# Kernel optimization log

Hardware: AMD Instinct MI355X
Metric: run time of the kernel (lower is better)

## Reference

```python
import jax, jax.numpy as jnp
import numpy as np


def toeplitz_from(weight_matrix):
    # Faithful to the torch Toeplitz parametrization:
    # parameters = concat(W[::-1, 0], W[0, 1:]); toep[i, j] = parameters[n_rows-1-i+j]
    n_rows, n_cols = weight_matrix.shape
    params = jnp.concatenate([weight_matrix[::-1, 0], weight_matrix[0, 1:]])
    idx = (n_rows - 1) - jnp.arange(n_rows)[:, None] + jnp.arange(n_cols)[None, :]
    return params[idx]  # [n_rows, n_cols], built in one gather instead of a loop


def setup_inputs() -> dict:
    key = jax.random.key(0)
    ks = jax.random.split(key, 8)
    B, frame_dim, esn_dim, last_dim = 65536, 64, 960, 1024
    comb = frame_dim + esn_dim
    s1 = 1.0 / np.sqrt(comb)
    s2 = 1.0 / np.sqrt(last_dim)
    return {
        "x_frame": jax.random.normal(ks[0], (B, frame_dim), jnp.float32),
        "h_esn": jax.random.normal(ks[1], (B, esn_dim), jnp.float32),
        "W1": jax.random.normal(ks[2], (last_dim, comb), jnp.float32) * s1,
        "b1": jax.random.normal(ks[3], (last_dim,), jnp.float32) * s1,
        "W_slope": jax.random.normal(ks[4], (frame_dim, last_dim), jnp.float32) * s2,
        "b_slope": jax.random.normal(ks[5], (frame_dim,), jnp.float32) * s2,
        "W_int": jax.random.normal(ks[6], (frame_dim, last_dim), jnp.float32) * s2,
        "b_int": jax.random.normal(ks[7], (frame_dim,), jnp.float32) * s2,
    }


def reference(x_frame, h_esn, W1, b1, W_slope, b_slope, W_int, b_int):
    W1_toep = toeplitz_from(W1)                      # [last_dim, frame+esn]
    combined = jnp.concatenate([x_frame, h_esn], axis=-1)  # [B, frame+esn]
    q_last = jax.nn.relu(combined @ W1_toep.T + b1)  # [B, last_dim]
    slope = jnp.tanh(q_last @ W_slope.T + b_slope)   # [B, frame_dim]
    intercept = q_last @ W_int.T + b_int             # [B, frame_dim]
    return slope, intercept
```

## Files before the change

### kernel.cpp

```cpp
#include <hip/hip_runtime.h>
#include <cstdint>
#include <cstddef>

typedef __bf16 bf16x8v __attribute__((ext_vector_type(8)));
typedef float f32x4v __attribute__((ext_vector_type(4)));

__device__ __forceinline__ void gload_lds16(const void* g, void* l) {
  __builtin_amdgcn_global_load_lds((const __attribute__((address_space(1))) void*)g,
                                   (__attribute__((address_space(3))) void*)l,
                                   16, 0, 0);
}

__device__ __forceinline__ bf16x8v cvt_bf16x8(f32x4v a, f32x4v b) {
  bf16x8v r;
  r[0] = (__bf16)a[0]; r[1] = (__bf16)a[1]; r[2] = (__bf16)a[2]; r[3] = (__bf16)a[3];
  r[4] = (__bf16)b[0]; r[5] = (__bf16)b[1]; r[6] = (__bf16)b[2]; r[7] = (__bf16)b[3];
  return r;
}

__global__ __launch_bounds__(256) void params_kernel(const float* __restrict__ W1,
                                                     float* __restrict__ params) {
  int p = blockIdx.x * 256 + threadIdx.x;
  if (p < 2047)
    params[p] = (p < 1024) ? W1[(size_t)(1023 - p) << 10] : W1[p - 1023];
}

__global__ __launch_bounds__(256) void pack_kernel(const float* __restrict__ x,
                                                   const float* __restrict__ h,
                                                   const float* __restrict__ params,
                                                   const float* __restrict__ Ws,
                                                   const float* __restrict__ Wi,
                                                   __bf16* __restrict__ Acat,
                                                   __bf16* __restrict__ toep,
                                                   __bf16* __restrict__ Wcat) {
  long u = (long)blockIdx.x * 256 + threadIdx.x;
  if (u < 8388608L) {
    int r = (int)(u >> 7), cg = (int)(u & 127);
    const float* s = (cg < 8) ? x + (size_t)r * 64 + cg * 8
                              : h + (size_t)r * 960 + (cg - 8) * 8;
    f32x4v a = *(const f32x4v*)s, b = *(const f32x4v*)(s + 4);
    *(bf16x8v*)(Acat + ((size_t)r << 10) + cg * 8) = cvt_bf16x8(a, b);
  } else if (u < 8519680L) {
    long t = u - 8388608L;
    int i = (int)(t >> 7), j0 = (int)(t & 127) * 8;
    const float* s = params + (1023 - i + j0);
    bf16x8v o;
#pragma unroll
    for (int e = 0; e < 8; ++e) o[e] = (__bf16)s[e];
    *(bf16x8v*)(toep + ((size_t)i << 10) + j0) = o;
  } else {
    long t = u - 8519680L;
    int n = (int)(t >> 7), k0 = (int)(t & 127) * 8;
    const float* s = (n < 64) ? Ws + ((size_t)n << 10) + k0
                              : Wi + ((size_t)(n - 64) << 10) + k0;
    f32x4v a = *(const f32x4v*)s, b = *(const f32x4v*)(s + 4);
    *(bf16x8v*)(Wcat + ((size_t)n << 10) + k0) = cvt_bf16x8(a, b);
  }
}

__global__ __launch_bounds__(256) void gemm1_dma(const __bf16* __restrict__ Acat,
                                                 const __bf16* __restrict__ toep,
                                                 const float* __restrict__ b1,
                                                 __bf16* __restrict__ q) {
  __shared__ __align__(16) __bf16 Ab0[128 * 32], Ab1[128 * 32];
  __shared__ __align__(16) __bf16 Bb0[128 * 32], Bb1[128 * 32];
  const int tid = threadIdx.x, wid = tid >> 6, lane = tid & 63;
  const int wrow = wid >> 1, wcol = wid & 1;
  const int bid = blockIdx.x;
  const int xcd = bid & 7, j = bid >> 3;
  const int m0 = (((j >> 3) << 3) | xcd) << 7;
  const int n0 = (j & 7) << 7;
  const int quad = lane >> 4, l15 = lane & 15;
  const int rl = lane >> 2, seg = lane & 3;

  f32x4v acc[4][4] = {};

  const __bf16* gA = Acat + (((size_t)(m0 + wid * 32 + rl)) << 10) + seg * 8;
  const __bf16* gB = toep + (((size_t)(n0 + wid * 32 + rl)) << 10) + seg * 8;
  const size_t ROW16 = (size_t)16 << 10;

  auto stage = [&](__bf16* la, __bf16* lb) {
    int rb = wid * 32;
    gload_lds16(gA,         &la[rb * 32]);
    gload_lds16(gA + ROW16, &la[(rb + 16) * 32]);
    gload_lds16(gB,         &lb[rb * 32]);
    gload_lds16(gB + ROW16, &lb[(rb + 16) * 32]);
    gA += 32; gB += 32;
  };

  auto compute = [&](const __bf16* la, const __bf16* lb) {
    bf16x8v af[4], bfr[4];
#pragma unroll
    for (int r = 0; r < 4; ++r)
      af[r] = *(const bf16x8v*)&la[(wrow * 64 + r * 16 + l15) * 32 + quad * 8];
#pragma unroll
    for (int c = 0; c < 4; ++c)
      bfr[c] = *(const bf16x8v*)&lb[(wcol * 64 + c * 16 + l15) * 32 + quad * 8];
#pragma unroll
    for (int r = 0; r < 4; ++r)
#pragma unroll
      for (int c = 0; c < 4; ++c)
        acc[r][c] = __builtin_amdgcn_mfma_f32_16x16x32_bf16(af[r], bfr[c], acc[r][c], 0, 0, 0);
  };

  stage(Ab0, Bb0);
  for (int kt = 0; kt < 32; kt += 2) {
    __syncthreads();
    stage(Ab1, Bb1);
    compute(Ab0, Bb0);
    __syncthreads();
    if (kt < 30) stage(Ab0, Bb0);
    compute(Ab1, Bb1);
  }

#pragma unroll
  for (int c = 0; c < 4; ++c) {
    int col = n0 + wcol * 64 + c * 16 + l15;
    float bias = b1[col];
#pragma unroll
    for (int r = 0; r < 4; ++r)
#pragma unroll
      for (int e = 0; e < 4; ++e) {
        int row = m0 + wrow * 64 + r * 16 + quad * 4 + e;
        q[((size_t)row << 10) + col] = (__bf16)fmaxf(acc[r][c][e] + bias, 0.0f);
      }
  }
}

__global__ __launch_bounds__(256) void gemm2_dma(const __bf16* __restrict__ q,
                                                 const __bf16* __restrict__ Wcat,
                                                 const float* __restrict__ b_slope,
                                                 const float* __restrict__ b_int,
                                                 float* __restrict__ out) {
  __shared__ __align__(16) __bf16 Ab[2][64 * 64];
  __shared__ __align__(16) __bf16 Bb[2][128 * 64];
  const int tid = threadIdx.x, wid = tid >> 6, lane = tid & 63;
  const int wrow = wid >> 1, wcol = wid & 1;
  const int m0 = blockIdx.x << 6;
  const int quad = lane >> 4, l15 = lane & 15;
  const int r8 = lane >> 3, s8 = lane & 7;

  f32x4v acc[2][4] = {};

  auto stage = [&](int buf, int kt) {
    int k0 = kt << 6;
#pragma unroll
    for (int j = 0; j < 2; ++j) {
      int rb = wid * 16 + j * 8;
      gload_lds16(q + (((size_t)(m0 + rb + r8)) << 10) + k0 + s8 * 8, &Ab[buf][rb * 64]);
    }
#pragma unroll
    for (int j = 0; j < 4; ++j) {
      int rb = wid * 32 + j * 8;
      gload_lds16(Wcat + (((size_t)(rb + r8)) << 10) + k0 + s8 * 8, &Bb[buf][rb * 64]);
    }
  };

  stage(0, 0);
  for (int kt = 0; kt < 16; ++kt) {
    int cur = kt & 1;
    __syncthreads();
    if (kt < 15) stage(cur ^ 1, kt + 1);
#pragma unroll
    for (int s = 0; s < 2; ++s) {
      bf16x8v af[2], bfr[4];
#pragma unroll
      for (int r = 0; r < 2; ++r)
        af[r] = *(const bf16x8v*)&Ab[cur][(wrow * 32 + r * 16 + l15) * 64 + s * 32 + quad * 8];
#pragma unroll
      for (int c = 0; c < 4; ++c)
        bfr[c] = *(const bf16x8v*)&Bb[cur][(wcol * 64 + c * 16 + l15) * 64 + s * 32 + quad * 8];
#pragma unroll
      for (int r = 0; r < 2; ++r)
#pragma unroll
        for (int c = 0; c < 4; ++c)
          acc[r][c] = __builtin_amdgcn_mfma_f32_16x16x32_bf16(af[r], bfr[c], acc[r][c], 0, 0, 0);
    }
  }

#pragma unroll
  for (int c = 0; c < 4; ++c) {
    int col = wcol * 64 + c * 16 + l15;
    float bias = (col < 64) ? b_slope[col] : b_int[col - 64];
#pragma unroll
    for (int r = 0; r < 2; ++r)
#pragma unroll
      for (int e = 0; e < 4; ++e) {
        int row = m0 + wrow * 32 + r * 16 + quad * 4 + e;
        float v = acc[r][c][e] + bias;
        if (col < 64) {
          float xc = fminf(fmaxf(v, -15.f), 15.f);
          float t = __expf(2.f * xc);
          out[(size_t)row * 64 + col] = (t - 1.f) / (t + 1.f);
        } else {
          out[(size_t)4194304 + (size_t)row * 64 + (col - 64)] = v;
        }
      }
  }
}

__global__ __launch_bounds__(256) void gemm1_fused(const float* __restrict__ x,
                                                   const float* __restrict__ h,
                                                   const __bf16* __restrict__ toep,
                                                   const float* __restrict__ b1,
                                                   __bf16* __restrict__ q) {
  __shared__ __align__(16) __bf16 At[128 * 32];
  __shared__ __align__(16) __bf16 Bt[128 * 32];
  const int tid = threadIdx.x, wid = tid >> 6, lane = tid & 63;
  const int wrow = wid >> 1, wcol = wid & 1;
  const int m0 = (blockIdx.x >> 3) << 7;
  const int n0 = (blockIdx.x & 7) << 7;
  const int quad = lane >> 4, l15 = lane & 15;
  const int rl = lane >> 2, seg = lane & 3;

  f32x4v acc[4][4] = {};
  auto a_ptr = [&](int k0, int t) -> const f32x4v* {
    const float* s; int ld, kk;
    if (k0 < 64) { s = x; ld = 64; kk = k0; } else { s = h; ld = 960; kk = k0 - 64; }
    int row = m0 + wid * 32 + t * 16 + rl;
    return (const f32x4v*)(s + (size_t)row * ld + kk + seg * 8);
  };
  f32x4v pv[2][2];
  { const f32x4v* p0 = a_ptr(0, 0); pv[0][0] = p0[0]; pv[0][1] = p0[1];
    const f32x4v* p1 = a_ptr(0, 1); pv[1][0] = p1[0]; pv[1][1] = p1[1]; }

  for (int k0 = 0; k0 < 1024; k0 += 32) {
    __syncthreads();
    { int rb = wid * 32;
#pragma unroll
      for (int c = 0; c < 2; ++c) {
        int row = rb + c * 16 + rl;
        gload_lds16(toep + (((size_t)(n0 + row)) << 10) + k0 + seg * 8, &Bt[(rb + c * 16) * 32]);
      } }
#pragma unroll
    for (int t = 0; t < 2; ++t) {
      int row = wid * 32 + t * 16 + rl;
      *(bf16x8v*)&At[row * 32 + seg * 8] = cvt_bf16x8(pv[t][0], pv[t][1]);
    }
    __syncthreads();
    if (k0 + 32 < 1024) {
      const f32x4v* p0 = a_ptr(k0 + 32, 0); f32x4v n00 = p0[0], n01 = p0[1];
      const f32x4v* p1 = a_ptr(k0 + 32, 1); f32x4v n10 = p1[0], n11 = p1[1];
      pv[0][0] = n00; pv[0][1] = n01; pv[1][0] = n10; pv[1][1] = n11;
    }
    bf16x8v af[4], bfr[4];
#pragma unroll
    for (int r = 0; r < 4; ++r)
      af[r] = *(const bf16x8v*)&At[(wrow * 64 + r * 16 + l15) * 32 + quad * 8];
#pragma unroll
    for (int c = 0; c < 4; ++c)
      bfr[c] = *(const bf16x8v*)&Bt[(wcol * 64 + c * 16 + l15) * 32 + quad * 8];
#pragma unroll
    for (int r = 0; r < 4; ++r)
#pragma unroll
      for (int c = 0; c < 4; ++c)
        acc[r][c] = __builtin_amdgcn_mfma_f32_16x16x32_bf16(af[r], bfr[c], acc[r][c], 0, 0, 0);
  }
#pragma unroll
  for (int c = 0; c < 4; ++c) {
    int col = n0 + wcol * 64 + c * 16 + l15;
    float bias = b1[col];
#pragma unroll
    for (int r = 0; r < 4; ++r)
#pragma unroll
      for (int e = 0; e < 4; ++e) {
        int row = m0 + wrow * 64 + r * 16 + quad * 4 + e;
        q[((size_t)row << 10) + col] = (__bf16)fmaxf(acc[r][c][e] + bias, 0.0f);
      }
  }
}

__global__ __launch_bounds__(256) void prep_kernel(const float* __restrict__ W1,
                                                   const float* __restrict__ Wslope,
                                                   const float* __restrict__ Wint,
                                                   __bf16* __restrict__ toep,
                                                   __bf16* __restrict__ Wcat) {
  int id = blockIdx.x * 256 + threadIdx.x;
  if (id < 1024 * 1024) {
    int i = id >> 10, j = id & 1023;
    int p = 1023 - i + j;
    float v = (p < 1024) ? W1[(size_t)(1023 - p) << 10] : W1[p - 1023];
    toep[id] = (__bf16)v;
  } else {
    int id2 = id - 1024 * 1024;
    int n = id2 >> 10, k = id2 & 1023;
    float v = (n < 64) ? Wslope[((size_t)n << 10) + k] : Wint[((size_t)(n - 64) << 10) + k];
    Wcat[id2] = (__bf16)v;
  }
}

extern "C" void kernel_launch(void* const* d_in, const int* in_sizes, int n_in,
                              void* d_out, int out_size, void* d_ws, size_t ws_size,
                              hipStream_t stream) {
  const float* x  = (const float*)d_in[0];
  const float* h  = (const float*)d_in[1];
  const float* W1 = (const float*)d_in[2];
  const float* b1 = (const float*)d_in[3];
  const float* Ws = (const float*)d_in[4];
  const float* bs = (const float*)d_in[5];
  const float* Wi = (const float*)d_in[6];
  const float* bi = (const float*)d_in[7];
  char* ws = (char*)d_ws;

  const size_t SZ_Q    = 134217728;
  const size_t SZ_ACAT = 134217728;
  const size_t SZ_TOEP = 2097152;
  const size_t SZ_WCAT = 262144;
  const size_t need = SZ_Q + SZ_ACAT + SZ_TOEP + SZ_WCAT + 8192;

  __bf16* q = (__bf16*)ws;
  if (ws_size >= need) {
    __bf16* Acat  = (__bf16*)(ws + SZ_Q);
    __bf16* toep  = (__bf16*)(ws + SZ_Q + SZ_ACAT);
    __bf16* Wcat  = (__bf16*)(ws + SZ_Q + SZ_ACAT + SZ_TOEP);
    float* params = (float*)(ws + SZ_Q + SZ_ACAT + SZ_TOEP + SZ_WCAT);
    hipLaunchKernelGGL(params_kernel, dim3(8),     dim3(256), 0, stream, W1, params);
    hipLaunchKernelGGL(pack_kernel,   dim3(33344), dim3(256), 0, stream,
                       x, h, params, Ws, Wi, Acat, toep, Wcat);
    hipLaunchKernelGGL(gemm1_dma,     dim3(4096),  dim3(256), 0, stream, Acat, toep, b1, q);
    hipLaunchKernelGGL(gemm2_dma,     dim3(1024),  dim3(256), 0, stream, q, Wcat, bs, bi,
                       (float*)d_out);
  } else {
    __bf16* toep = (__bf16*)(ws + SZ_Q);
    __bf16* Wcat = (__bf16*)(ws + SZ_Q + SZ_TOEP);
    hipLaunchKernelGGL(prep_kernel,   dim3(4608), dim3(256), 0, stream, W1, Ws, Wi, toep, Wcat);
    hipLaunchKernelGGL(gemm1_fused,   dim3(4096), dim3(256), 0, stream, x, h, toep, b1, q);
    hipLaunchKernelGGL(gemm2_dma,     dim3(1024), dim3(256), 0, stream, q, Wcat, bs, bi,
                       (float*)d_out);
  }
}
```

Measured before the change: 607.7 us.

## Stream fp32 activations directly into LDS in gemm1 and drop the bf16 pack pass

Removes the separate pass that converted x and h into a bf16 Acat buffer. gemm1 now DMAs fp32 activation tiles straight into double-buffered LDS and converts them to bf16 when loading MFMA fragments. It also XOR-swizzles the LDS layouts in gemm1 and gemm2 to reduce bank conflicts. This saves a full 128MB write and read of Acat, at the cost of double the LDS footprint for A tiles and extra conversion work inside the inner loop.

```diff
diff --git a/kernel.cpp b/kernel.cpp
--- a/kernel.cpp
+++ b/kernel.cpp
@@ -16,258 +16,6 @@
   r[0] = (__bf16)a[0]; r[1] = (__bf16)a[1]; r[2] = (__bf16)a[2]; r[3] = (__bf16)a[3];
   r[4] = (__bf16)b[0]; r[5] = (__bf16)b[1]; r[6] = (__bf16)b[2]; r[7] = (__bf16)b[3];
   return r;
-}
-
-__global__ __launch_bounds__(256) void params_kernel(const float* __restrict__ W1,
-                                                     float* __restrict__ params) {
-  int p = blockIdx.x * 256 + threadIdx.x;
-  if (p < 2047)
-    params[p] = (p < 1024) ? W1[(size_t)(1023 - p) << 10] : W1[p - 1023];
-}
-
-__global__ __launch_bounds__(256) void pack_kernel(const float* __restrict__ x,
-                                                   const float* __restrict__ h,
-                                                   const float* __restrict__ params,
-                                                   const float* __restrict__ Ws,
-                                                   const float* __restrict__ Wi,
-                                                   __bf16* __restrict__ Acat,
-                                                   __bf16* __restrict__ toep,
-                                                   __bf16* __restrict__ Wcat) {
-  long u = (long)blockIdx.x * 256 + threadIdx.x;
-  if (u < 8388608L) {
-    int r = (int)(u >> 7), cg = (int)(u & 127);
-    const float* s = (cg < 8) ? x + (size_t)r * 64 + cg * 8
-                              : h + (size_t)r * 960 + (cg - 8) * 8;
-    f32x4v a = *(const f32x4v*)s, b = *(const f32x4v*)(s + 4);
-    *(bf16x8v*)(Acat + ((size_t)r << 10) + cg * 8) = cvt_bf16x8(a, b);
-  } else if (u < 8519680L) {
-    long t = u - 8388608L;
-    int i = (int)(t >> 7), j0 = (int)(t & 127) * 8;
-    const float* s = params + (1023 - i + j0);
-    bf16x8v o;
-#pragma unroll
-    for (int e = 0; e < 8; ++e) o[e] = (__bf16)s[e];
-    *(bf16x8v*)(toep + ((size_t)i << 10) + j0) = o;
-  } else {
-    long t = u - 8519680L;
-    int n = (int)(t >> 7), k0 = (int)(t & 127) * 8;
-    const float* s = (n < 64) ? Ws + ((size_t)n << 10) + k0
-                              : Wi + ((size_t)(n - 64) << 10) + k0;
-    f32x4v a = *(const f32x4v*)s, b = *(const f32x4v*)(s + 4);
-    *(bf16x8v*)(Wcat + ((size_t)n << 10) + k0) = cvt_bf16x8(a, b);
-  }
-}
-
-__global__ __launch_bounds__(256) void gemm1_dma(const __bf16* __restrict__ Acat,
-                                                 const __bf16* __restrict__ toep,
-                                                 const float* __restrict__ b1,
-                                                 __bf16* __restrict__ q) {
-  __shared__ __align__(16) __bf16 Ab0[128 * 32], Ab1[128 * 32];
-  __shared__ __align__(16) __bf16 Bb0[128 * 32], Bb1[128 * 32];
-  const int tid = threadIdx.x, wid = tid >> 6, lane = tid & 63;
-  const int wrow = wid >> 1, wcol = wid & 1;
-  const int bid = blockIdx.x;
-  const int xcd = bid & 7, j = bid >> 3;
-  const int m0 = (((j >> 3) << 3) | xcd) << 7;
-  const int n0 = (j & 7) << 7;
-  const int quad = lane >> 4, l15 = lane & 15;
-  const int rl = lane >> 2, seg = lane & 3;
-
-  f32x4v acc[4][4] = {};
-
-  const __bf16* gA = Acat + (((size_t)(m0 + wid * 32 + rl)) << 10) + seg * 8;
-  const __bf16* gB = toep + (((size_t)(n0 + wid * 32 + rl)) << 10) + seg * 8;
-  const size_t ROW16 = (size_t)16 << 10;
-
-  auto stage = [&](__bf16* la, __bf16* lb) {
-    int rb = wid * 32;
-    gload_lds16(gA,         &la[rb * 32]);
-    gload_lds16(gA + ROW16, &la[(rb + 16) * 32]);
-    gload_lds16(gB,         &lb[rb * 32]);
-    gload_lds16(gB + ROW16, &lb[(rb + 16) * 32]);
-    gA += 32; gB += 32;
-  };
-
-  auto compute = [&](const __bf16* la, const __bf16* lb) {
-    bf16x8v af[4], bfr[4];
-#pragma unroll
-    for (int r = 0; r < 4; ++r)
-      af[r] = *(const bf16x8v*)&la[(wrow * 64 + r * 16 + l15) * 32 + quad * 8];
-#pragma unroll
-    for (int c = 0; c < 4; ++c)
-      bfr[c] = *(const bf16x8v*)&lb[(wcol * 64 + c * 16 + l15) * 32 + quad * 8];
-#pragma unroll
-    for (int r = 0; r < 4; ++r)
-#pragma unroll
-      for (int c = 0; c < 4; ++c)
-        acc[r][c] = __builtin_amdgcn_mfma_f32_16x16x32_bf16(af[r], bfr[c], acc[r][c], 0, 0, 0);
-  };
-
-  stage(Ab0, Bb0);
-  for (int kt = 0; kt < 32; kt += 2) {
-    __syncthreads();
-    stage(Ab1, Bb1);
-    compute(Ab0, Bb0);
-    __syncthreads();
-    if (kt < 30) stage(Ab0, Bb0);
-    compute(Ab1, Bb1);
-  }
-
-#pragma unroll
-  for (int c = 0; c < 4; ++c) {
-    int col = n0 + wcol * 64 + c * 16 + l15;
-    float bias = b1[col];
-#pragma unroll
-    for (int r = 0; r < 4; ++r)
-#pragma unroll
-      for (int e = 0; e < 4; ++e) {
-        int row = m0 + wrow * 64 + r * 16 + quad * 4 + e;
-        q[((size_t)row << 10) + col] = (__bf16)fmaxf(acc[r][c][e] + bias, 0.0f);
-      }
-  }
-}
-
-__global__ __launch_bounds__(256) void gemm2_dma(const __bf16* __restrict__ q,
-                                                 const __bf16* __restrict__ Wcat,
-                                                 const float* __restrict__ b_slope,
-                                                 const float* __restrict__ b_int,
-                                                 float* __restrict__ out) {
-  __shared__ __align__(16) __bf16 Ab[2][64 * 64];
-  __shared__ __align__(16) __bf16 Bb[2][128 * 64];
-  const int tid = threadIdx.x, wid = tid >> 6, lane = tid & 63;
-  const int wrow = wid >> 1, wcol = wid & 1;
-  const int m0 = blockIdx.x << 6;
-  const int quad = lane >> 4, l15 = lane & 15;
-  const int r8 = lane >> 3, s8 = lane & 7;
-
-  f32x4v acc[2][4] = {};
-
-  auto stage = [&](int buf, int kt) {
-    int k0 = kt << 6;
-#pragma unroll
-    for (int j = 0; j < 2; ++j) {
-      int rb = wid * 16 + j * 8;
-      gload_lds16(q + (((size_t)(m0 + rb + r8)) << 10) + k0 + s8 * 8, &Ab[buf][rb * 64]);
-    }
-#pragma unroll
-    for (int j = 0; j < 4; ++j) {
-      int rb = wid * 32 + j * 8;
-      gload_lds16(Wcat + (((size_t)(rb + r8)) << 10) + k0 + s8 * 8, &Bb[buf][rb * 64]);
-    }
-  };
-
-  stage(0, 0);
-  for (int kt = 0; kt < 16; ++kt) {
-    int cur = kt & 1;
-    __syncthreads();
-    if (kt < 15) stage(cur ^ 1, kt + 1);
-#pragma unroll
-    for (int s = 0; s < 2; ++s) {
-      bf16x8v af[2], bfr[4];
-#pragma unroll
-      for (int r = 0; r < 2; ++r)
-        af[r] = *(const bf16x8v*)&Ab[cur][(wrow * 32 + r * 16 + l15) * 64 + s * 32 + quad * 8];
-#pragma unroll
-      for (int c = 0; c < 4; ++c)
-        bfr[c] = *(const bf16x8v*)&Bb[cur][(wcol * 64 + c * 16 + l15) * 64 + s * 32 + quad * 8];
-#pragma unroll
-      for (int r = 0; r < 2; ++r)
-#pragma unroll
-        for (int c = 0; c < 4; ++c)
-          acc[r][c] = __builtin_amdgcn_mfma_f32_16x16x32_bf16(af[r], bfr[c], acc[r][c], 0, 0, 0);
-    }
-  }
-
-#pragma unroll
-  for (int c = 0; c < 4; ++c) {
-    int col = wcol * 64 + c * 16 + l15;
-    float bias = (col < 64) ? b_slope[col] : b_int[col - 64];
-#pragma unroll
-    for (int r = 0; r < 2; ++r)
-#pragma unroll
-      for (int e = 0; e < 4; ++e) {
-        int row = m0 + wrow * 32 + r * 16 + quad * 4 + e;
-        float v = acc[r][c][e] + bias;
-        if (col < 64) {
-          float xc = fminf(fmaxf(v, -15.f), 15.f);
-          float t = __expf(2.f * xc);
-          out[(size_t)row * 64 + col] = (t - 1.f) / (t + 1.f);
-        } else {
-          out[(size_t)4194304 + (size_t)row * 64 + (col - 64)] = v;
-        }
-      }
-  }
-}
-
-__global__ __launch_bounds__(256) void gemm1_fused(const float* __restrict__ x,
-                                                   const float* __restrict__ h,
-                                                   const __bf16* __restrict__ toep,
-                                                   const float* __restrict__ b1,
-                                                   __bf16* __restrict__ q) {
-  __shared__ __align__(16) __bf16 At[128 * 32];
-  __shared__ __align__(16) __bf16 Bt[128 * 32];
-  const int tid = threadIdx.x, wid = tid >> 6, lane = tid & 63;
-  const int wrow = wid >> 1, wcol = wid & 1;
-  const int m0 = (blockIdx.x >> 3) << 7;
-  const int n0 = (blockIdx.x & 7) << 7;
-  const int quad = lane >> 4, l15 = lane & 15;
-  const int rl = lane >> 2, seg = lane & 3;
-
-  f32x4v acc[4][4] = {};
-  auto a_ptr = [&](int k0, int t) -> const f32x4v* {
-    const float* s; int ld, kk;
-    if (k0 < 64) { s = x; ld = 64; kk = k0; } else { s = h; ld = 960; kk = k0 - 64; }
-    int row = m0 + wid * 32 + t * 16 + rl;
-    return (const f32x4v*)(s + (size_t)row * ld + kk + seg * 8);
-  };
-  f32x4v pv[2][2];
-  { const f32x4v* p0 = a_ptr(0, 0); pv[0][0] = p0[0]; pv[0][1] = p0[1];
-    const f32x4v* p1 = a_ptr(0, 1); pv[1][0] = p1[0]; pv[1][1] = p1[1]; }
-
-  for (int k0 = 0; k0 < 1024; k0 += 32) {
-    __syncthreads();
-    { int rb = wid * 32;
-#pragma unroll
-      for (int c = 0; c < 2; ++c) {
-        int row = rb + c * 16 + rl;
-        gload_lds16(toep + (((size_t)(n0 + row)) << 10) + k0 + seg * 8, &Bt[(rb + c * 16) * 32]);
-      } }
-#pragma unroll
-    for (int t = 0; t < 2; ++t) {
-      int row = wid * 32 + t * 16 + rl;
-      *(bf16x8v*)&At[row * 32 + seg * 8] = cvt_bf16x8(pv[t][0], pv[t][1]);
-    }
-    __syncthreads();
-    if (k0 + 32 < 1024) {
-      const f32x4v* p0 = a_ptr(k0 + 32, 0); f32x4v n00 = p0[0], n01 = p0[1];
-      const f32x4v* p1 = a_ptr(k0 + 32, 1); f32x4v n10 = p1[0], n11 = p1[1];
-      pv[0][0] = n00; pv[0][1] = n01; pv[1][0] = n10; pv[1][1] = n11;
-    }
-    bf16x8v af[4], bfr[4];
-#pragma unroll
-    for (int r = 0; r < 4; ++r)
-      af[r] = *(const bf16x8v*)&At[(wrow * 64 + r * 16 + l15) * 32 + quad * 8];
-#pragma unroll
-    for (int c = 0; c < 4; ++c)
-      bfr[c] = *(const bf16x8v*)&Bt[(wcol * 64 + c * 16 + l15) * 32 + quad * 8];
-#pragma unroll
-    for (int r = 0; r < 4; ++r)
-#pragma unroll
-      for (int c = 0; c < 4; ++c)
-        acc[r][c] = __builtin_amdgcn_mfma_f32_16x16x32_bf16(af[r], bfr[c], acc[r][c], 0, 0, 0);
-  }
-#pragma unroll
-  for (int c = 0; c < 4; ++c) {
-    int col = n0 + wcol * 64 + c * 16 + l15;
-    float bias = b1[col];
-#pragma unroll
-    for (int r = 0; r < 4; ++r)
-#pragma unroll
-      for (int e = 0; e < 4; ++e) {
-        int row = m0 + wrow * 64 + r * 16 + quad * 4 + e;
-        q[((size_t)row << 10) + col] = (__bf16)fmaxf(acc[r][c][e] + bias, 0.0f);
-      }
-  }
 }
 
 __global__ __launch_bounds__(256) void prep_kernel(const float* __restrict__ W1,
@@ -289,6 +37,175 @@
   }
 }
 
+__global__ __launch_bounds__(256) void gemm1_f32dma(const float* __restrict__ x,
+                                                    const float* __restrict__ h,
+                                                    const __bf16* __restrict__ toep,
+                                                    const float* __restrict__ b1,
+                                                    __bf16* __restrict__ q) {
+  __shared__ __align__(16) float  Af[2][128 * 32];
+  __shared__ __align__(16) __bf16 Bf[2][128 * 32];
+  const int tid = threadIdx.x, wid = tid >> 6, lane = tid & 63;
+  const int wrow = wid >> 1, wcol = wid & 1;
+  const int bid = blockIdx.x;
+  const int xcd = bid & 7, j = bid >> 3;
+  const int m0 = (((j >> 3) << 3) | xcd) << 7;
+  const int n0 = (j & 7) << 7;
+  const int quad = lane >> 4, l15 = lane & 15;
+  const int rl8 = lane >> 3, s8 = lane & 7;
+  const int sA = s8 ^ rl8;
+  const int rl4 = lane >> 2, s4 = lane & 3;
+  const int sB = s4 ^ (rl4 & 3);
+
+  f32x4v acc[4][4] = {};
+
+  const int arow = m0 + wid * 32;
+  const __bf16* gB = toep + (((size_t)(n0 + wid * 32 + rl4)) << 10) + sB * 8;
+  const size_t BROW16 = (size_t)16 << 10;
+
+  auto stageA = [&](float* la, int kt) {
+    const int k0 = kt << 5;
+    const float* src;
+    int rstride;
+    if (k0 < 64) { src = x + (size_t)(arow + rl8) * 64 + k0 + sA * 4;        rstride = 8 * 64; }
+    else         { src = h + (size_t)(arow + rl8) * 960 + (k0 - 64) + sA * 4; rstride = 8 * 960; }
+    const int rb = wid * 32;
+#pragma unroll
+    for (int i = 0; i < 4; ++i) {
+      gload_lds16(src, &la[(rb + i * 8) * 32]);
+      src += rstride;
+    }
+  };
+  auto stageB = [&](__bf16* lb) {
+    const int rb = wid * 32;
+    gload_lds16(gB,          &lb[rb * 32]);
+    gload_lds16(gB + BROW16, &lb[(rb + 16) * 32]);
+    gB += 32;
+  };
+
+  auto compute = [&](const float* la, const __bf16* lb) {
+    bf16x8v af[4], bfr[4];
+#pragma unroll
+    for (int r = 0; r < 4; ++r) {
+      const int row = wrow * 64 + r * 16 + l15;
+      const f32x4v* base = (const f32x4v*)&la[row * 32];
+      f32x4v lo = base[(quad * 2)     ^ (row & 7)];
+      f32x4v hi = base[(quad * 2 + 1) ^ (row & 7)];
+      af[r] = cvt_bf16x8(lo, hi);
+    }
+#pragma unroll
+    for (int c = 0; c < 4; ++c) {
+      const int row = wcol * 64 + c * 16 + l15;
+      const bf16x8v* bb = (const bf16x8v*)&lb[row * 32];
+      bfr[c] = bb[quad ^ (row & 3)];
+    }
+#pragma unroll
+    for (int r = 0; r < 4; ++r)
+#pragma unroll
+      for (int c = 0; c < 4; ++c)
+        acc[r][c] = __builtin_amdgcn_mfma_f32_16x16x32_bf16(af[r], bfr[c], acc[r][c], 0, 0, 0);
+  };
+
+  stageA(Af[0], 0); stageB(Bf[0]);
+  for (int kt = 0; kt < 32; kt += 2) {
+    __syncthreads();
+    stageA(Af[1], kt + 1); stageB(Bf[1]);
+    compute(Af[0], Bf[0]);
+    __syncthreads();
+    if (kt < 30) { stageA(Af[0], kt + 2); stageB(Bf[0]); }
+    compute(Af[1], Bf[1]);
+  }
+
+#pragma unroll
+  for (int c = 0; c < 4; ++c) {
+    int col = n0 + wcol * 64 + c * 16 + l15;
+    float bias = b1[col];
+#pragma unroll
+    for (int r = 0; r < 4; ++r)
+#pragma unroll
+      for (int e = 0; e < 4; ++e) {
+        int row = m0 + wrow * 64 + r * 16 + quad * 4 + e;
+        q[((size_t)row << 10) + col] = (__bf16)fmaxf(acc[r][c][e] + bias, 0.0f);
+      }
+  }
+}
+
+__global__ __launch_bounds__(256) void gemm2_dma(const __bf16* __restrict__ q,
+                                                 const __bf16* __restrict__ Wcat,
+                                                 const float* __restrict__ b_slope,
+                                                 const float* __restrict__ b_int,
+                                                 float* __restrict__ out) {
+  __shared__ __align__(16) __bf16 Ab[2][64 * 64];
+  __shared__ __align__(16) __bf16 Bb[2][128 * 64];
+  const int tid = threadIdx.x, wid = tid >> 6, lane = tid & 63;
+  const int wrow = wid >> 1, wcol = wid & 1;
+  const int m0 = blockIdx.x << 6;
+  const int quad = lane >> 4, l15 = lane & 15;
+  const int r8 = lane >> 3, s8 = lane & 7;
+  const int sw = (s8 ^ r8) * 8;
+
+  f32x4v acc[2][4] = {};
+
+  auto stage = [&](int buf, int kt) {
+    int k0 = kt << 6;
+#pragma unroll
+    for (int j2 = 0; j2 < 2; ++j2) {
+      int rb = wid * 16 + j2 * 8;
+      gload_lds16(q + (((size_t)(m0 + rb + r8)) << 10) + k0 + sw, &Ab[buf][rb * 64]);
+    }
+#pragma unroll
+    for (int j2 = 0; j2 < 4; ++j2) {
+      int rb = wid * 32 + j2 * 8;
+      gload_lds16(Wcat + (((size_t)(rb + r8)) << 10) + k0 + sw, &Bb[buf][rb * 64]);
+    }
+  };
+
+  stage(0, 0);
+  for (int kt = 0; kt < 16; ++kt) {
+    int cur = kt & 1;
+    __syncthreads();
+    if (kt < 15) stage(cur ^ 1, kt + 1);
+#pragma unroll
+    for (int s = 0; s < 2; ++s) {
+      bf16x8v af[2], bfr[4];
+#pragma unroll
+      for (int r = 0; r < 2; ++r) {
+        const int row = wrow * 32 + r * 16 + l15;
+        af[r] = *(const bf16x8v*)&Ab[cur][row * 64 + (((s * 4 + quad) ^ (row & 7)) * 8)];
+      }
+#pragma unroll
+      for (int c = 0; c < 4; ++c) {
+        const int row = wcol * 64 + c * 16 + l15;
+        bfr[c] = *(const bf16x8v*)&Bb[cur][row * 64 + (((s * 4 + quad) ^ (row & 7)) * 8)];
+      }
+#pragma unroll
+      for (int r = 0; r < 2; ++r)
+#pragma unroll
+        for (int c = 0; c < 4; ++c)
+          acc[r][c] = __builtin_amdgcn_mfma_f32_16x16x32_bf16(af[r], bfr[c], acc[r][c], 0, 0, 0);
+    }
+  }
+
+#pragma unroll
+  for (int c = 0; c < 4; ++c) {
+    int col = wcol * 64 + c * 16 + l15;
+    float bias = (col < 64) ? b_slope[col] : b_int[col - 64];
+#pragma unroll
+    for (int r = 0; r < 2; ++r)
+#pragma unroll
+      for (int e = 0; e < 4; ++e) {
+        int row = m0 + wrow * 32 + r * 16 + quad * 4 + e;
+        float v = acc[r][c][e] + bias;
+        if (col < 64) {
+          float xc = fminf(fmaxf(v, -15.f), 15.f);
+          float t = __expf(2.f * xc);
+          out[(size_t)row * 64 + col] = (t - 1.f) / (t + 1.f);
+        } else {
+          out[(size_t)4194304 + (size_t)row * 64 + (col - 64)] = v;
+        }
+      }
+  }
+}
+
 extern "C" void kernel_launch(void* const* d_in, const int* in_sizes, int n_in,
                               void* d_out, int out_size, void* d_ws, size_t ws_size,
                               hipStream_t stream) {
@@ -303,29 +220,14 @@
   char* ws = (char*)d_ws;
 
   const size_t SZ_Q    = 134217728;
-  const size_t SZ_ACAT = 134217728;
   const size_t SZ_TOEP = 2097152;
-  const size_t SZ_WCAT = 262144;
-  const size_t need = SZ_Q + SZ_ACAT + SZ_TOEP + SZ_WCAT + 8192;
-
-  __bf16* q = (__bf16*)ws;
-  if (ws_size >= need) {
-    __bf16* Acat  = (__bf16*)(ws + SZ_Q);
-    __bf16* toep  = (__bf16*)(ws + SZ_Q + SZ_ACAT);
-    __bf16* Wcat  = (__bf16*)(ws + SZ_Q + SZ_ACAT + SZ_TOEP);
-    float* params = (float*)(ws + SZ_Q + SZ_ACAT + SZ_TOEP + SZ_WCAT);
-    hipLaunchKernelGGL(params_kernel, dim3(8),     dim3(256), 0, stream, W1, params);
-    hipLaunchKernelGGL(pack_kernel,   dim3(33344), dim3(256), 0, stream,
-                       x, h, params, Ws, Wi, Acat, toep, Wcat);
-    hipLaunchKernelGGL(gemm1_dma,     dim3(4096),  dim3(256), 0, stream, Acat, toep, b1, q);
-    hipLaunchKernelGGL(gemm2_dma,     dim3(1024),  dim3(256), 0, stream, q, Wcat, bs, bi,
-                       (float*)d_out);
-  } else {
-    __bf16* toep = (__bf16*)(ws + SZ_Q);
-    __bf16* Wcat = (__bf16*)(ws + SZ_Q + SZ_TOEP);
-    hipLaunchKernelGGL(prep_kernel,   dim3(4608), dim3(256), 0, stream, W1, Ws, Wi, toep, Wcat);
-    hipLaunchKernelGGL(gemm1_fused,   dim3(4096), dim3(256), 0, stream, x, h, toep, b1, q);
-    hipLaunchKernelGGL(gemm2_dma,     dim3(1024), dim3(256), 0, stream, q, Wcat, bs, bi,
-                       (float*)d_out);
-  }
-}
+
+  __bf16* q    = (__bf16*)ws;
+  __bf16* toep = (__bf16*)(ws + SZ_Q);
+  __bf16* Wcat = (__bf16*)(ws + SZ_Q + SZ_TOEP);
+
+  hipLaunchKernelGGL(prep_kernel,  dim3(4608), dim3(256), 0, stream, W1, Ws, Wi, toep, Wcat);
+  hipLaunchKernelGGL(gemm1_f32dma, dim3(4096), dim3(256), 0, stream, x, h, toep, b1, q);
+  hipLaunchKernelGGL(gemm2_dma,    dim3(1024), dim3(256), 0, stream, q, Wcat, bs, bi,
+                     (float*)d_out);
+}
```

Result: no change. 612.6 us (+0.8%).
